# Performance work log

Hardware: AMD Instinct MI355X
Metric: run time of the kernel (lower is better)

The kernel has to match this reference:

```python
import jax, jax.numpy as jnp
import numpy as np

BS, DIM = 8192, 768
TEMPERATURE = 1.0
EPS = 1e-8


def setup_inputs() -> dict:
    key = jax.random.key(0)
    k1, k2 = jax.random.split(key)
    text_emb = jax.random.normal(k1, (BS, DIM), dtype=jnp.float32)
    ctr_emb = jax.random.normal(k2, (BS, DIM), dtype=jnp.float32)
    return {"text_emb": text_emb, "ctr_emb": ctr_emb}


def _l2norm(x):
    # cosine scorer normalization
    return x / jnp.maximum(jnp.linalg.norm(x, axis=-1, keepdims=True), EPS)


def reference(text_emb, ctr_emb):
    t = _l2norm(text_emb)          # [bs, d]
    c = _l2norm(ctr_emb)           # [bs, d]
    # S[i, j] = cos(text_i, ctr_j) / T  -- single GEMM instead of (bs,bs,d) broadcast
    S = jnp.einsum('id,jd->ij', t, c) / TEMPERATURE   # [bs, bs]
    sim_ii = jnp.diagonal(S)                           # [bs]
    # loss1_i = lse_j S[i,j] - S[i,i]; loss2_i = lse_j S[j,i] - S[i,i]
    loss = (jax.nn.logsumexp(S, axis=1)
            + jax.nn.logsumexp(S, axis=0)
            - 2.0 * sim_ii)
    return jnp.mean(loss)
```

## Files before the change

kernel.cpp:

```cpp
#include <hip/hip_runtime.h>
#include <hip/hip_bf16.h>

#define BS   8192
#define DIM  768
#define TILE 128
#define BK   128

typedef float f32x4 __attribute__((ext_vector_type(4)));
typedef int   i32x4 __attribute__((ext_vector_type(4)));
typedef int   i32x8 __attribute__((ext_vector_type(8)));

__device__ __forceinline__ void async16(const void* g, void* l) {
    __builtin_amdgcn_global_load_lds(
        (const __attribute__((address_space(1))) unsigned int*)g,
        (__attribute__((address_space(3))) unsigned int*)l,
        16, 0, 0);
}

__global__ __launch_bounds__(256) void normalize_kernel(
    const float* __restrict__ text, const float* __restrict__ ctr,
    unsigned char* __restrict__ tq, unsigned char* __restrict__ cq,
    float* __restrict__ sim) {
    const int lane = threadIdx.x & 63;
    const int row  = blockIdx.x * 4 + (threadIdx.x >> 6);
    const size_t base = (size_t)row * DIM;

    float4 t[3], c[3];
    float st = 0.f, sc = 0.f, sd = 0.f;
#pragma unroll
    for (int i = 0; i < 3; ++i) {
        t[i] = *(const float4*)&text[base + lane * 4 + i * 256];
        c[i] = *(const float4*)&ctr [base + lane * 4 + i * 256];
        st += t[i].x*t[i].x + t[i].y*t[i].y + t[i].z*t[i].z + t[i].w*t[i].w;
        sc += c[i].x*c[i].x + c[i].y*c[i].y + c[i].z*c[i].z + c[i].w*c[i].w;
        sd += t[i].x*c[i].x + t[i].y*c[i].y + t[i].z*c[i].z + t[i].w*c[i].w;
    }
#pragma unroll
    for (int off = 1; off < 64; off <<= 1) {
        st += __shfl_xor(st, off);
        sc += __shfl_xor(sc, off);
        sd += __shfl_xor(sd, off);
    }
    const float invt = 1.0f / fmaxf(sqrtf(st), 1e-8f);
    const float invc = 1.0f / fmaxf(sqrtf(sc), 1e-8f);
#pragma unroll
    for (int i = 0; i < 3; ++i) {
        unsigned int wt = (unsigned int)__builtin_amdgcn_cvt_pk_fp8_f32(t[i].x * invt, t[i].y * invt, 0, false);
        wt = (unsigned int)__builtin_amdgcn_cvt_pk_fp8_f32(t[i].z * invt, t[i].w * invt, (int)wt, true);
        unsigned int wcq = (unsigned int)__builtin_amdgcn_cvt_pk_fp8_f32(c[i].x * invc, c[i].y * invc, 0, false);
        wcq = (unsigned int)__builtin_amdgcn_cvt_pk_fp8_f32(c[i].z * invc, c[i].w * invc, (int)wcq, true);
        *(unsigned int*)&tq[base + lane * 4 + i * 256] = wt;
        *(unsigned int*)&cq[base + lane * 4 + i * 256] = wcq;
    }
    if (lane == 0) sim[row] = sd * invt * invc;
}

__global__ __launch_bounds__(256) void gemm_lse_kernel(
    const unsigned char* __restrict__ tq, const unsigned char* __restrict__ cq,
    float* __restrict__ rowsum, float* __restrict__ colsum) {
    __shared__ char ldsA[TILE * BK];
    __shared__ char ldsB[TILE * BK];

    const int tid = threadIdx.x;

    const int bid = blockIdx.x;
    const int xcd = bid & 7, idx = bid >> 3;
    const int tileCol = idx >> 3, rowInBand = idx & 7;
    const int rowBase = (xcd * 8 + rowInBand) * TILE;
    const int colBase = tileCol * TILE;

    const int wave = tid >> 6, lane = tid & 63;
    const int wr = wave >> 1, wc = wave & 1;
    const int quad = lane >> 4, l16 = lane & 15;

    int goff[4];
    char *dstA[4], *dstB[4];
#pragma unroll
    for (int i = 0; i < 4; ++i) {
        const int p  = tid + i * 256;
        const int kc = p >> 8;
        const int row = (p >> 1) & 127;
        const int hl  = (p & 1) ^ (kc & 1);
        goff[i] = row * DIM + kc * 32 + hl * 16;
        dstA[i] = ldsA + p * 16;
        dstB[i] = ldsB + p * 16;
    }
    const unsigned char* gA = tq + (size_t)rowBase * DIM;
    const unsigned char* gB = cq + (size_t)colBase * DIM;

    const int sw = quad & 1;
    int aoff[4], boff[4];
#pragma unroll
    for (int mt = 0; mt < 4; ++mt) aoff[mt] = quad * 4096 + (wr * 64 + mt * 16 + l16) * 32;
#pragma unroll
    for (int nt = 0; nt < 4; ++nt) boff[nt] = quad * 4096 + (wc * 64 + nt * 16 + l16) * 32;

    f32x4 acc[4][4];
#pragma unroll
    for (int mt = 0; mt < 4; ++mt)
#pragma unroll
        for (int nt = 0; nt < 4; ++nt)
            acc[mt][nt] = (f32x4){0.f, 0.f, 0.f, 0.f};

    for (int k0 = 0; k0 < DIM; k0 += BK) {
#pragma unroll
        for (int i = 0; i < 4; ++i) {
            async16(gA + goff[i] + k0, dstA[i]);
            async16(gB + goff[i] + k0, dstB[i]);
        }
        __syncthreads();

        i32x8 af[4], bf[4];
#pragma unroll
        for (int mt = 0; mt < 4; ++mt) {
            i32x4 lo = *(const i32x4*)(ldsA + aoff[mt] + sw * 16);
            i32x4 hi = *(const i32x4*)(ldsA + aoff[mt] + (sw ^ 1) * 16);
            af[mt] = __builtin_shufflevector(lo, hi, 0, 1, 2, 3, 4, 5, 6, 7);
        }
#pragma unroll
        for (int nt = 0; nt < 4; ++nt) {
            i32x4 lo = *(const i32x4*)(ldsB + boff[nt] + sw * 16);
            i32x4 hi = *(const i32x4*)(ldsB + boff[nt] + (sw ^ 1) * 16);
            bf[nt] = __builtin_shufflevector(lo, hi, 0, 1, 2, 3, 4, 5, 6, 7);
        }

#pragma unroll
        for (int mt = 0; mt < 4; ++mt)
#pragma unroll
            for (int nt = 0; nt < 4; ++nt)
                acc[mt][nt] = __builtin_amdgcn_mfma_scale_f32_16x16x128_f8f6f4(
                    af[mt], bf[nt], acc[mt][nt], 0, 0, 0, 127, 0, 127);
        __syncthreads();
    }

    float rp[4][4];
    float cp[4];
#pragma unroll
    for (int mt = 0; mt < 4; ++mt)
#pragma unroll
        for (int r = 0; r < 4; ++r) rp[mt][r] = 0.f;
#pragma unroll
    for (int nt = 0; nt < 4; ++nt) cp[nt] = 0.f;

#pragma unroll
    for (int mt = 0; mt < 4; ++mt)
#pragma unroll
        for (int nt = 0; nt < 4; ++nt)
#pragma unroll
            for (int r = 0; r < 4; ++r) {
                const float e = __expf(acc[mt][nt][r]);
                rp[mt][r] += e;
                cp[nt]    += e;
            }

#pragma unroll
    for (int mt = 0; mt < 4; ++mt)
#pragma unroll
        for (int r = 0; r < 4; ++r) {
            float v = rp[mt][r];
            v += __shfl_xor(v, 1);
            v += __shfl_xor(v, 2);
            v += __shfl_xor(v, 4);
            v += __shfl_xor(v, 8);
            rp[mt][r] = v;
        }
    if (l16 == 0) {
#pragma unroll
        for (int mt = 0; mt < 4; ++mt)
#pragma unroll
            for (int r = 0; r < 4; ++r)
                atomicAdd(&rowsum[rowBase + wr * 64 + mt * 16 + quad * 4 + r], rp[mt][r]);
    }
#pragma unroll
    for (int nt = 0; nt < 4; ++nt) {
        float v = cp[nt];
        v += __shfl_xor(v, 16);
        v += __shfl_xor(v, 32);
        if (quad == 0)
            atomicAdd(&colsum[colBase + wc * 64 + nt * 16 + l16], v);
    }
}

__global__ __launch_bounds__(256) void finalize_kernel(
    const float* __restrict__ rowsum, const float* __restrict__ colsum,
    const float* __restrict__ sim, float* __restrict__ out) {
    const int tid = threadIdx.x;
    float acc = 0.f;
    for (int i = tid; i < BS; i += 256)
        acc += logf(rowsum[i]) + logf(colsum[i]) - 2.f * sim[i];
#pragma unroll
    for (int off = 1; off < 64; off <<= 1) acc += __shfl_xor(acc, off);
    __shared__ float red[4];
    const int wave = tid >> 6, lane = tid & 63;
    if (lane == 0) red[wave] = acc;
    __syncthreads();
    if (tid == 0) out[0] = (red[0] + red[1] + red[2] + red[3]) / (float)BS;
}

extern "C" void kernel_launch(void* const* d_in, const int* in_sizes, int n_in,
                              void* d_out, int out_size, void* d_ws, size_t ws_size,
                              hipStream_t stream) {
    const float* text = (const float*)d_in[0];
    const float* ctr  = (const float*)d_in[1];

    char* ws = (char*)d_ws;
    const size_t embBytes = (size_t)BS * DIM;
    unsigned char* tq = (unsigned char*)ws;
    unsigned char* cq = (unsigned char*)(ws + embBytes);
    float* sim    = (float*)(ws + 2 * embBytes);
    float* rowsum = (float*)(ws + 2 * embBytes + BS * sizeof(float));
    float* colsum = (float*)(ws + 2 * embBytes + 2 * BS * sizeof(float));

    hipMemsetAsync(rowsum, 0, 2 * BS * sizeof(float), stream);

    normalize_kernel<<<BS / 4, 256, 0, stream>>>(text, ctr, tq, cq, sim);

    gemm_lse_kernel<<<(BS / TILE) * (BS / TILE), 256, 0, stream>>>(tq, cq, rowsum, colsum);

    finalize_kernel<<<1, 256, 0, stream>>>(rowsum, colsum, sim, (float*)d_out);
}
```

Before: 204.9 us.

## Use 512-thread GEMM blocks, fold memset into normalize, widen finalize

```diff
diff --git a/kernel.cpp b/kernel.cpp
--- a/kernel.cpp
+++ b/kernel.cpp
@@ -20,7 +20,12 @@
 __global__ __launch_bounds__(256) void normalize_kernel(
     const float* __restrict__ text, const float* __restrict__ ctr,
     unsigned char* __restrict__ tq, unsigned char* __restrict__ cq,
-    float* __restrict__ sim) {
+    float* __restrict__ sim, float* __restrict__ rowsum, float* __restrict__ colsum) {
+    if (blockIdx.x < 64) {
+        const int i = blockIdx.x * 256 + threadIdx.x;
+        rowsum[i] = 0.f;
+        colsum[i] = 0.f;
+    }
     const int lane = threadIdx.x & 63;
     const int row  = blockIdx.x * 4 + (threadIdx.x >> 6);
     const size_t base = (size_t)row * DIM;
@@ -55,7 +60,7 @@
     if (lane == 0) sim[row] = sd * invt * invc;
 }
 
-__global__ __launch_bounds__(256) void gemm_lse_kernel(
+__global__ __launch_bounds__(512, 4) void gemm_lse_kernel(
     const unsigned char* __restrict__ tq, const unsigned char* __restrict__ cq,
     float* __restrict__ rowsum, float* __restrict__ colsum) {
     __shared__ char ldsA[TILE * BK];
@@ -70,14 +75,14 @@
     const int colBase = tileCol * TILE;
 
     const int wave = tid >> 6, lane = tid & 63;
-    const int wr = wave >> 1, wc = wave & 1;
+    const int wr = wave >> 2, wc = wave & 3;
     const int quad = lane >> 4, l16 = lane & 15;
 
-    int goff[4];
-    char *dstA[4], *dstB[4];
-#pragma unroll
-    for (int i = 0; i < 4; ++i) {
-        const int p  = tid + i * 256;
+    int goff[2];
+    char *dstA[2], *dstB[2];
+#pragma unroll
+    for (int i = 0; i < 2; ++i) {
+        const int p  = tid + i * 512;
         const int kc = p >> 8;
         const int row = (p >> 1) & 127;
         const int hl  = (p & 1) ^ (kc & 1);
@@ -89,63 +94,60 @@
     const unsigned char* gB = cq + (size_t)colBase * DIM;
 
     const int sw = quad & 1;
-    int aoff[4], boff[4];
+    int aoff[4], boff[2];
 #pragma unroll
     for (int mt = 0; mt < 4; ++mt) aoff[mt] = quad * 4096 + (wr * 64 + mt * 16 + l16) * 32;
 #pragma unroll
-    for (int nt = 0; nt < 4; ++nt) boff[nt] = quad * 4096 + (wc * 64 + nt * 16 + l16) * 32;
-
-    f32x4 acc[4][4];
-#pragma unroll
-    for (int mt = 0; mt < 4; ++mt)
-#pragma unroll
-        for (int nt = 0; nt < 4; ++nt)
+    for (int nt = 0; nt < 2; ++nt) boff[nt] = quad * 4096 + (wc * 32 + nt * 16 + l16) * 32;
+
+    f32x4 acc[4][2];
+#pragma unroll
+    for (int mt = 0; mt < 4; ++mt)
+#pragma unroll
+        for (int nt = 0; nt < 2; ++nt)
             acc[mt][nt] = (f32x4){0.f, 0.f, 0.f, 0.f};
 
     for (int k0 = 0; k0 < DIM; k0 += BK) {
 #pragma unroll
-        for (int i = 0; i < 4; ++i) {
+        for (int i = 0; i < 2; ++i) {
             async16(gA + goff[i] + k0, dstA[i]);
             async16(gB + goff[i] + k0, dstB[i]);
         }
         __syncthreads();
 
-        i32x8 af[4], bf[4];
+        i32x8 bf[2];
+#pragma unroll
+        for (int nt = 0; nt < 2; ++nt) {
+            i32x4 lo = *(const i32x4*)(ldsB + boff[nt] + sw * 16);
+            i32x4 hi = *(const i32x4*)(ldsB + boff[nt] + (sw ^ 1) * 16);
+            bf[nt] = __builtin_shufflevector(lo, hi, 0, 1, 2, 3, 4, 5, 6, 7);
+        }
 #pragma unroll
         for (int mt = 0; mt < 4; ++mt) {
             i32x4 lo = *(const i32x4*)(ldsA + aoff[mt] + sw * 16);
             i32x4 hi = *(const i32x4*)(ldsA + aoff[mt] + (sw ^ 1) * 16);
-            af[mt] = __builtin_shufflevector(lo, hi, 0, 1, 2, 3, 4, 5, 6, 7);
-        }
-#pragma unroll
-        for (int nt = 0; nt < 4; ++nt) {
-            i32x4 lo = *(const i32x4*)(ldsB + boff[nt] + sw * 16);
-            i32x4 hi = *(const i32x4*)(ldsB + boff[nt] + (sw ^ 1) * 16);
-            bf[nt] = __builtin_shufflevector(lo, hi, 0, 1, 2, 3, 4, 5, 6, 7);
-        }
-
-#pragma unroll
-        for (int mt = 0; mt < 4; ++mt)
-#pragma unroll
-            for (int nt = 0; nt < 4; ++nt)
+            i32x8 af = __builtin_shufflevector(lo, hi, 0, 1, 2, 3, 4, 5, 6, 7);
+#pragma unroll
+            for (int nt = 0; nt < 2; ++nt)
                 acc[mt][nt] = __builtin_amdgcn_mfma_scale_f32_16x16x128_f8f6f4(
-                    af[mt], bf[nt], acc[mt][nt], 0, 0, 0, 127, 0, 127);
+                    af, bf[nt], acc[mt][nt], 0, 0, 0, 127, 0, 127);
+        }
         __syncthreads();
     }
 
     float rp[4][4];
-    float cp[4];
+    float cp[2];
 #pragma unroll
     for (int mt = 0; mt < 4; ++mt)
 #pragma unroll
         for (int r = 0; r < 4; ++r) rp[mt][r] = 0.f;
 #pragma unroll
-    for (int nt = 0; nt < 4; ++nt) cp[nt] = 0.f;
-
-#pragma unroll
-    for (int mt = 0; mt < 4; ++mt)
-#pragma unroll
-        for (int nt = 0; nt < 4; ++nt)
+    for (int nt = 0; nt < 2; ++nt) cp[nt] = 0.f;
+
+#pragma unroll
+    for (int mt = 0; mt < 4; ++mt)
+#pragma unroll
+        for (int nt = 0; nt < 2; ++nt)
 #pragma unroll
             for (int r = 0; r < 4; ++r) {
                 const float e = __expf(acc[mt][nt][r]);
@@ -172,29 +174,42 @@
                 atomicAdd(&rowsum[rowBase + wr * 64 + mt * 16 + quad * 4 + r], rp[mt][r]);
     }
 #pragma unroll
-    for (int nt = 0; nt < 4; ++nt) {
+    for (int nt = 0; nt < 2; ++nt) {
         float v = cp[nt];
         v += __shfl_xor(v, 16);
         v += __shfl_xor(v, 32);
         if (quad == 0)
-            atomicAdd(&colsum[colBase + wc * 64 + nt * 16 + l16], v);
-    }
-}
-
-__global__ __launch_bounds__(256) void finalize_kernel(
+            atomicAdd(&colsum[colBase + wc * 32 + nt * 16 + l16], v);
+    }
+}
+
+__global__ __launch_bounds__(1024) void finalize_kernel(
     const float* __restrict__ rowsum, const float* __restrict__ colsum,
     const float* __restrict__ sim, float* __restrict__ out) {
     const int tid = threadIdx.x;
     float acc = 0.f;
-    for (int i = tid; i < BS; i += 256)
-        acc += logf(rowsum[i]) + logf(colsum[i]) - 2.f * sim[i];
+#pragma unroll
+    for (int i = 0; i < 2; ++i) {
+        const int j = (tid + i * 1024) * 4;
+        float4 rs = *(const float4*)&rowsum[j];
+        float4 cs = *(const float4*)&colsum[j];
+        float4 sm = *(const float4*)&sim[j];
+        acc += __logf(rs.x) + __logf(rs.y) + __logf(rs.z) + __logf(rs.w);
+        acc += __logf(cs.x) + __logf(cs.y) + __logf(cs.z) + __logf(cs.w);
+        acc -= 2.f * (sm.x + sm.y + sm.z + sm.w);
+    }
 #pragma unroll
     for (int off = 1; off < 64; off <<= 1) acc += __shfl_xor(acc, off);
-    __shared__ float red[4];
+    __shared__ float red[16];
     const int wave = tid >> 6, lane = tid & 63;
     if (lane == 0) red[wave] = acc;
     __syncthreads();
-    if (tid == 0) out[0] = (red[0] + red[1] + red[2] + red[3]) / (float)BS;
+    if (tid == 0) {
+        float s = 0.f;
+#pragma unroll
+        for (int w = 0; w < 16; ++w) s += red[w];
+        out[0] = s / (float)BS;
+    }
 }
 
 extern "C" void kernel_launch(void* const* d_in, const int* in_sizes, int n_in,
@@ -211,11 +226,9 @@
     float* rowsum = (float*)(ws + 2 * embBytes + BS * sizeof(float));
     float* colsum = (float*)(ws + 2 * embBytes + 2 * BS * sizeof(float));
 
-    hipMemsetAsync(rowsum, 0, 2 * BS * sizeof(float), stream);
-
-    normalize_kernel<<<BS / 4, 256, 0, stream>>>(text, ctr, tq, cq, sim);
-
-    gemm_lse_kernel<<<(BS / TILE) * (BS / TILE), 256, 0, stream>>>(tq, cq, rowsum, colsum);
-
-    finalize_kernel<<<1, 256, 0, stream>>>(rowsum, colsum, sim, (float*)d_out);
-}
+    normalize_kernel<<<BS / 4, 256, 0, stream>>>(text, ctr, tq, cq, sim, rowsum, colsum);
+
+    gemm_lse_kernel<<<(BS / TILE) * (BS / TILE), 512, 0, stream>>>(tq, cq, rowsum, colsum);
+
+    finalize_kernel<<<1, 1024, 0, stream>>>(rowsum, colsum, sim, (float*)d_out);
+}
```

New measurement: 195.8 us. 4.4% less time.
